# Kernel optimization log

Hardware: AMD Instinct MI355X
Metric: run time of the kernel (lower is better)

The kernel has to match this reference:

```python
import jax, jax.numpy as jnp
import numpy as np

B, G, S, NNZ = 64, 20000, 200000, 2000000

def setup_inputs() -> dict:
    key = jax.random.key(0)
    k1, k2, k3, k4, k5 = jax.random.split(key, 5)
    x = jax.random.normal(k1, (B, G), dtype=jnp.float32)
    # COO connectivity: row = SNP index (output), col = gene index (input)
    row = jax.random.randint(k2, (NNZ,), 0, S, dtype=jnp.int64)
    col = jax.random.randint(k3, (NNZ,), 0, G, dtype=jnp.int64)
    index = jnp.stack([row, col])  # [2, NNZ]
    W_sparse = jax.random.normal(k4, (NNZ,), dtype=jnp.float32) * 0.02
    b = jax.random.normal(k5, (S, 1), dtype=jnp.float32) * 0.02
    return {"x": x, "W_sparse": W_sparse, "b": b, "index": index, "n_SNPs": S}

def reference(x, W_sparse, b, index, n_SNPs):
    # spmm: sparse [n_SNPs, n_genes] @ x.T [n_genes, B] -> [n_SNPs, B]
    row, col = index[0], index[1]
    gathered = x.T[col] * W_sparse[:, None]            # [NNZ, B] edge contributions
    dot_prod = jax.ops.segment_sum(gathered, row, num_segments=n_SNPs)  # [S, B]
    output = dot_prod + b                              # bias broadcast over batch
    return output.T                                    # [B, n_SNPs]
```

## Files before the change

kernel.cpp:

```cpp
#include <hip/hip_runtime.h>


#define WAVE 64
#define CHUNK 8192
#define RBITS 6
#define BINROWS 64
#define SCAN_PAD 3584
#define CAP_BIN 896

#define RL(v, i)  __builtin_amdgcn_readlane((int)(v), (i))
#define RLF(v, i) __int_as_float(__builtin_amdgcn_readlane(__float_as_int(v), (i)))

__device__ __forceinline__ int swz(int r, int b) {
    return (r << 6) + (b ^ (r & 63));
}

__device__ __forceinline__ unsigned short f2bf(float f) {
    unsigned u = __float_as_uint(f);
    unsigned r = (u + 0x7fffu + ((u >> 16) & 1u)) >> 16;
    return (unsigned short)r;
}

__global__ void transpose64_kernel(const float* __restrict__ x,
                                   unsigned short* __restrict__ xTh, int G) {
    __shared__ float tile[64][65];
    const int t  = threadIdx.x;
    const int g0 = blockIdx.x * 64;
    {
        const int j  = t & 63;
        const int b0 = t >> 6;
        if (g0 + j < G) {
            #pragma unroll
            for (int it = 0; it < 16; ++it) {
                const int b = b0 + it * 4;
                tile[j][b] = x[(size_t)b * G + g0 + j];
            }
        }
    }
    __syncthreads();
    {
        const int b  = t & 63;
        const int j0 = t >> 6;
        #pragma unroll
        for (int it = 0; it < 16; ++it) {
            const int j = j0 + it * 4;
            if (g0 + j < G) xTh[(size_t)(g0 + j) * WAVE + b] = f2bf(tile[j][b]);
        }
    }
}

__global__ __launch_bounds__(512) void pass1_kernel(
        const int* __restrict__ row, const int* __restrict__ col,
        const float* __restrict__ w, uint2* __restrict__ sedge1,
        unsigned* __restrict__ segtab, int nnz, int nbin) {
    __shared__ __align__(16) uint2 stage[CHUNK];
    __shared__ int hist[SCAN_PAD];
    __shared__ int wpart[8];
    const int t    = threadIdx.x;
    const int lane = t & 63;
    const int wv   = t >> 6;
    const int e0   = blockIdx.x * CHUNK;
    const bool full = (e0 + CHUNK <= nnz);
    const int M    = full ? CHUNK : (nnz - e0);

    for (int j = t; j < SCAN_PAD; j += 512) hist[j] = 0;
    __syncthreads();

    if (full) {
        const int4* rv = (const int4*)(row + e0);
        #pragma unroll
        for (int k = 0; k < CHUNK / 2048; ++k) {
            const int4 r4 = rv[k * 512 + t];
            atomicAdd(&hist[r4.x >> RBITS], 1);
            atomicAdd(&hist[r4.y >> RBITS], 1);
            atomicAdd(&hist[r4.z >> RBITS], 1);
            atomicAdd(&hist[r4.w >> RBITS], 1);
        }
    } else {
        for (int k = 0; k < CHUNK / 512; ++k) {
            const int i = k * 512 + t;
            if (i < M) atomicAdd(&hist[row[e0 + i] >> RBITS], 1);
        }
    }
    __syncthreads();

    int c[7];
    int p = 0;
    #pragma unroll
    for (int j = 0; j < 7; ++j) { c[j] = hist[t * 7 + j]; p += c[j]; }
    int incl = p;
    #pragma unroll
    for (int d = 1; d < 64; d <<= 1) {
        const int u = __shfl_up(incl, d);
        if (lane >= d) incl += u;
    }
    if (lane == 63) wpart[wv] = incl;
    __syncthreads();
    int base = incl - p;
    #pragma unroll
    for (int ww = 0; ww < 8; ++ww)
        if (ww < wv) base += wpart[ww];
    unsigned* st = segtab + (size_t)blockIdx.x * (size_t)(nbin + 1);
    int run = base;
    #pragma unroll
    for (int j = 0; j < 7; ++j) {
        const int bj = t * 7 + j;
        hist[bj] = run;
        if (bj <= nbin) st[bj] = (unsigned)(e0 + run);
        run += c[j];
    }
    __syncthreads();

    if (full) {
        const int4*   rv = (const int4*)(row + e0);
        const int4*   cv = (const int4*)(col + e0);
        const float4* wf = (const float4*)(w + e0);
        #pragma unroll
        for (int k = 0; k < CHUNK / 2048; ++k) {
            const int4   r4 = rv[k * 512 + t];
            const int4   c4 = cv[k * 512 + t];
            const float4 w4 = wf[k * 512 + t];
            {
                const int pos = atomicAdd(&hist[r4.x >> RBITS], 1);
                stage[pos] = make_uint2(((unsigned)(r4.x & 63) << 15) |
                                        (unsigned)c4.x, __float_as_uint(w4.x));
            }
            {
                const int pos = atomicAdd(&hist[r4.y >> RBITS], 1);
                stage[pos] = make_uint2(((unsigned)(r4.y & 63) << 15) |
                                        (unsigned)c4.y, __float_as_uint(w4.y));
            }
            {
                const int pos = atomicAdd(&hist[r4.z >> RBITS], 1);
                stage[pos] = make_uint2(((unsigned)(r4.z & 63) << 15) |
                                        (unsigned)c4.z, __float_as_uint(w4.z));
            }
            {
                const int pos = atomicAdd(&hist[r4.w >> RBITS], 1);
                stage[pos] = make_uint2(((unsigned)(r4.w & 63) << 15) |
                                        (unsigned)c4.w, __float_as_uint(w4.w));
            }
        }
    } else {
        for (int k = 0; k < CHUNK / 512; ++k) {
            const int i = k * 512 + t;
            if (i < M) {
                const int r = row[e0 + i];
                const int pos = atomicAdd(&hist[r >> RBITS], 1);
                stage[pos] = make_uint2(((unsigned)(r & 63) << 15) |
                                        (unsigned)col[e0 + i],
                                        __float_as_uint(w[e0 + i]));
            }
        }
    }
    __syncthreads();

    {
        const uint4* sg4 = (const uint4*)stage;
        uint4* o4 = (uint4*)(sedge1 + e0);
        for (int j = t; j < (M >> 1); j += 512) o4[j] = sg4[j];
        if ((M & 1) && t == 0) sedge1[e0 + M - 1] = stage[M - 1];
    }
}

#define PROC(Er, ar, ii)                                                      \
    {                                                                         \
        const int   k_ = RL((Er).x, (ii));                                    \
        const float w_ = __int_as_float(RL((Er).y, (ii)));                    \
        const float v_ = __uint_as_float(                                     \
            (unsigned)*(const unsigned short*)(xb + k_ + lane2) << 16);       \
        (ar) += v_ * w_;                                                      \
    }

__global__ __launch_bounds__(256) void compute_kernel(
        const unsigned short* __restrict__ xTh,
        const uint2* __restrict__ sedge1,
        const unsigned* __restrict__ segtab,
        const float* __restrict__ bias,
        float* __restrict__ out, int S, int nchunk, int nbin) {
    __shared__ float tile[64 * 64];
    __shared__ uint2 eds2[CAP_BIN];
    __shared__ int   rcnt[4][BINROWS];
    __shared__ int   cur[4][BINROWS];
    __shared__ int   rstart[BINROWS], rend[BINROWS];
    __shared__ int   spart[4];
    uint2* eds1 = (uint2*)tile;

    const int t    = threadIdx.x;
    const int lane = t & 63;
    const int wv   = t >> 6;

    const int nwg = nbin;
    const int q8 = nwg >> 3, r8 = nwg & 7;
    const int xcd = (int)blockIdx.x & 7, off = (int)blockIdx.x >> 3;
    const int b = (xcd < r8 ? xcd * (q8 + 1) : r8 * (q8 + 1) + (xcd - r8) * q8)
                  + off;
    const int r0 = b << RBITS;

    if (t < BINROWS) {
        rcnt[0][t] = 0; rcnt[1][t] = 0; rcnt[2][t] = 0; rcnt[3][t] = 0;
    }

    int myst0 = 0, myn0 = 0, myst1 = 0, myn1 = 0;
    {
        const size_t stride = (size_t)(nbin + 1);
        if (t < nchunk) {
            const unsigned s = segtab[(size_t)t * stride + b];
            myn0  = (int)(segtab[(size_t)t * stride + b + 1] - s);
            myst0 = (int)s;
        }
        const int c2 = t + 256;
        if (c2 < nchunk) {
            const unsigned s = segtab[(size_t)c2 * stride + b];
            myn1  = (int)(segtab[(size_t)c2 * stride + b + 1] - s);
            myst1 = (int)s;
        }
    }
    const int nt = myn0 + myn1;
    int incl = nt;
    #pragma unroll
    for (int d = 1; d < 64; d <<= 1) {
        const int u = __shfl_up(incl, d);
        if (lane >= d) incl += u;
    }
    if (lane == 63) spart[wv] = incl;
    __syncthreads();
    int base = incl - nt;
    #pragma unroll
    for (int ww = 0; ww < 4; ++ww)
        if (ww < wv) base += spart[ww];
    int M = spart[0] + spart[1] + spart[2] + spart[3];
    if (M > CAP_BIN) M = CAP_BIN;

    for (int k = 0; k < myn0; ++k) {
        const int p = base + k;
        if (p < CAP_BIN) eds1[p] = sedge1[myst0 + k];
    }
    for (int k = 0; k < myn1; ++k) {
        const int p = base + myn0 + k;
        if (p < CAP_BIN) eds1[p] = sedge1[myst1 + k];
    }
    __syncthreads();

    for (int i = t; i < M; i += 256)
        atomicAdd(&rcnt[wv][eds1[i].x >> 15], 1);
    __syncthreads();

    if (t < BINROWS) {
        const int c0 = rcnt[0][t], c1 = rcnt[1][t];
        const int c2 = rcnt[2][t], c3 = rcnt[3][t];
        const int tot = c0 + c1 + c2 + c3;
        int inc2 = tot;
        #pragma unroll
        for (int d = 1; d < 64; d <<= 1) {
            const int u = __shfl_up(inc2, d);
            if (lane >= d) inc2 += u;
        }
        const int stt = inc2 - tot;
        rstart[t] = stt;
        rend[t]   = stt + tot;
        cur[0][t] = stt;
        cur[1][t] = stt + c0;
        cur[2][t] = stt + c0 + c1;
        cur[3][t] = stt + c0 + c1 + c2;
    }
    __syncthreads();

    for (int i = t; i < M; i += 256) {
        const uint2 e = eds1[i];
        const int r = (int)(e.x >> 15);
        const int pos = atomicAdd(&cur[wv][r], 1);
        eds2[pos] = make_uint2((e.x & 0x7fffu) << 7, e.y);
    }
    __syncthreads();

    const char* xb = (const char*)xTh;
    const int lane2 = lane * 2;
    const int rw = r0 + wv * 16;
    float bv = 0.f;
    if (lane < 16 && rw + lane < S) bv = bias[rw + lane];

    #pragma unroll
    for (int qd = 0; qd < 4; ++qd) {
        const int rl = wv * 16 + qd * 4;
        int s0 = rstart[rl + 0], e0g = rend[rl + 0];
        int s1 = rstart[rl + 1], e1g = rend[rl + 1];
        int s2 = rstart[rl + 2], e2g = rend[rl + 2];
        int s3 = rstart[rl + 3], e3g = rend[rl + 3];
        float a0 = 0.f, a1 = 0.f, a2 = 0.f, a3 = 0.f;
        while ((s0 < e0g) || (s1 < e1g) || (s2 < e2g) || (s3 < e3g)) {
            const int m0 = min(WAVE, e0g - s0);
            const int m1 = min(WAVE, e1g - s1);
            const int m2 = min(WAVE, e2g - s2);
            const int m3 = min(WAVE, e3g - s3);
            uint2 E0 = make_uint2(0u, 0u), E1 = make_uint2(0u, 0u);
            uint2 E2 = make_uint2(0u, 0u), E3 = make_uint2(0u, 0u);
            if (lane < m0) E0 = eds2[s0 + lane];
            if (lane < m1) E1 = eds2[s1 + lane];
            if (lane < m2) E2 = eds2[s2 + lane];
            if (lane < m3) E3 = eds2[s3 + lane];
            const int mm = max(max(m0, m1), max(m2, m3));
            int i = 0;
            for (; i + 2 <= mm; i += 2) {
                PROC(E0, a0, i) PROC(E1, a1, i) PROC(E2, a2, i) PROC(E3, a3, i)
                PROC(E0, a0, i + 1) PROC(E1, a1, i + 1)
                PROC(E2, a2, i + 1) PROC(E3, a3, i + 1)
            }
            if (i < mm) {
                PROC(E0, a0, i) PROC(E1, a1, i) PROC(E2, a2, i) PROC(E3, a3, i)
            }
            s0 += max(m0, 0); s1 += max(m1, 0);
            s2 += max(m2, 0); s3 += max(m3, 0);
        }
        tile[swz(rl + 0, lane)] = a0 + RLF(bv, qd * 4 + 0);
        tile[swz(rl + 1, lane)] = a1 + RLF(bv, qd * 4 + 1);
        tile[swz(rl + 2, lane)] = a2 + RLF(bv, qd * 4 + 2);
        tile[swz(rl + 3, lane)] = a3 + RLF(bv, qd * 4 + 3);
    }
    __syncthreads();

    const int srow = r0 + lane;
    #pragma unroll
    for (int k = 0; k < 16; ++k) {
        const int bb = wv * 16 + k;
        if (srow < S) out[(size_t)bb * S + srow] = tile[swz(lane, bb)];
    }
}

extern "C" void kernel_launch(void* const* d_in, const int* in_sizes, int n_in,
                              void* d_out, int out_size, void* d_ws, size_t ws_size,
                              hipStream_t stream) {
    const float* x    = (const float*)d_in[0];
    const float* W    = (const float*)d_in[1];
    const float* bias = (const float*)d_in[2];
    const int*   idx  = (const int*)d_in[3];

    const int NNZ = in_sizes[1];
    const int S   = in_sizes[2];
    const int B   = out_size / S;
    const int G   = in_sizes[0] / B;
    const int* rowi = idx;
    const int* coli = idx + NNZ;
    float* out = (float*)d_out;

    const int nbin   = (S + BINROWS - 1) >> RBITS;
    const int nchunk = (NNZ + CHUNK - 1) / CHUNK;

    char* ws = (char*)d_ws;
    size_t o = 0;
    auto alloc = [&](size_t bytes) {
        void* p = ws + o;
        o = (o + bytes + 255) & ~(size_t)255;
        return p;
    };
    unsigned short* xTh = (unsigned short*)alloc((size_t)G * B * sizeof(unsigned short));
    uint2*    sedge1 = (uint2*)   alloc((size_t)NNZ * sizeof(uint2));
    unsigned* segtab = (unsigned*)alloc((size_t)nchunk * (size_t)(nbin + 1) *
                                        sizeof(unsigned));
    (void)ws_size; (void)n_in;

    const int tgrid = (G + 63) / 64;
    transpose64_kernel<<<tgrid, 256, 0, stream>>>(x, xTh, G);

    pass1_kernel<<<nchunk, 512, 0, stream>>>(rowi, coli, W, sedge1, segtab,
                                             NNZ, nbin);
    compute_kernel<<<nbin, 256, 0, stream>>>(xTh, sedge1, segtab, bias,
                                             out, S, nchunk, nbin);
}
```

Measured before the change: 165.1 us.

## Fuse transpose and binning passes into one launch with smaller chunks

Merges the x transpose/bf16 conversion kernel and the edge-binning pass into a single prep kernel: the first blocks transpose and the rest bin edges, which removes one launch and lets the two run concurrently. Chunk size drops from 8192 to 2048 edges, with 256 threads per block and each thread keeping its row/col/weight loads in registers between the histogram and scatter phases. The result is four times as many chunks, so the compute kernel now reads up to four segment-table entries per thread and gathers from more, smaller segments. That adds scattered segtab reads and shorter copy loops in the compute stage.

```diff
diff --git a/kernel.cpp b/kernel.cpp
--- a/kernel.cpp
+++ b/kernel.cpp
@@ -2,11 +2,12 @@
 
 
 #define WAVE 64
-#define CHUNK 8192
+#define CHUNK 2048
 #define RBITS 6
 #define BINROWS 64
-#define SCAN_PAD 3584
+#define NBIN_PAD 3584
 #define CAP_BIN 896
+#define PREP_SMEM (CHUNK * 8 + NBIN_PAD * 4 + 16)
 
 #define RL(v, i)  __builtin_amdgcn_readlane((int)(v), (i))
 #define RLF(v, i) __int_as_float(__builtin_amdgcn_readlane(__float_as_int(v), (i)))
@@ -21,145 +22,138 @@
     return (unsigned short)r;
 }
 
-__global__ void transpose64_kernel(const float* __restrict__ x,
-                                   unsigned short* __restrict__ xTh, int G) {
-    __shared__ float tile[64][65];
-    const int t  = threadIdx.x;
-    const int g0 = blockIdx.x * 64;
-    {
-        const int j  = t & 63;
-        const int b0 = t >> 6;
-        if (g0 + j < G) {
-            #pragma unroll
-            for (int it = 0; it < 16; ++it) {
-                const int b = b0 + it * 4;
-                tile[j][b] = x[(size_t)b * G + g0 + j];
-            }
-        }
-    }
-    __syncthreads();
-    {
-        const int b  = t & 63;
-        const int j0 = t >> 6;
-        #pragma unroll
-        for (int it = 0; it < 16; ++it) {
-            const int j = j0 + it * 4;
-            if (g0 + j < G) xTh[(size_t)(g0 + j) * WAVE + b] = f2bf(tile[j][b]);
-        }
-    }
-}
-
-__global__ __launch_bounds__(512) void pass1_kernel(
+__global__ __launch_bounds__(256) void prep_kernel(
+        const float* __restrict__ x, unsigned short* __restrict__ xTh,
+        int G, int tgrid,
         const int* __restrict__ row, const int* __restrict__ col,
         const float* __restrict__ w, uint2* __restrict__ sedge1,
         unsigned* __restrict__ segtab, int nnz, int nbin) {
-    __shared__ __align__(16) uint2 stage[CHUNK];
-    __shared__ int hist[SCAN_PAD];
-    __shared__ int wpart[8];
-    const int t    = threadIdx.x;
+    __shared__ __align__(16) char smem[PREP_SMEM];
+    const int t = threadIdx.x;
+
+    if ((int)blockIdx.x < tgrid) {
+        float (*tile)[65] = (float (*)[65])smem;
+        const int g0 = blockIdx.x * 64;
+        {
+            const int j  = t & 63;
+            const int b0 = t >> 6;
+            if (g0 + j < G) {
+                #pragma unroll
+                for (int it = 0; it < 16; ++it) {
+                    const int b = b0 + it * 4;
+                    tile[j][b] = x[(size_t)b * G + g0 + j];
+                }
+            }
+        }
+        __syncthreads();
+        {
+            const int b  = t & 63;
+            const int j0 = t >> 6;
+            #pragma unroll
+            for (int it = 0; it < 16; ++it) {
+                const int j = j0 + it * 4;
+                if (g0 + j < G) xTh[(size_t)(g0 + j) * WAVE + b] = f2bf(tile[j][b]);
+            }
+        }
+        return;
+    }
+
+    uint2* stage = (uint2*)smem;
+    int*   hist  = (int*)(smem + CHUNK * 8);
+    int*   wpart = (int*)(smem + CHUNK * 8 + NBIN_PAD * 4);
     const int lane = t & 63;
     const int wv   = t >> 6;
-    const int e0   = blockIdx.x * CHUNK;
+    const int blk  = (int)blockIdx.x - tgrid;
+    const int e0   = blk * CHUNK;
     const bool full = (e0 + CHUNK <= nnz);
     const int M    = full ? CHUNK : (nnz - e0);
 
-    for (int j = t; j < SCAN_PAD; j += 512) hist[j] = 0;
-    __syncthreads();
-
-    if (full) {
-        const int4* rv = (const int4*)(row + e0);
-        #pragma unroll
-        for (int k = 0; k < CHUNK / 2048; ++k) {
-            const int4 r4 = rv[k * 512 + t];
-            atomicAdd(&hist[r4.x >> RBITS], 1);
-            atomicAdd(&hist[r4.y >> RBITS], 1);
-            atomicAdd(&hist[r4.z >> RBITS], 1);
-            atomicAdd(&hist[r4.w >> RBITS], 1);
-        }
-    } else {
-        for (int k = 0; k < CHUNK / 512; ++k) {
-            const int i = k * 512 + t;
-            if (i < M) atomicAdd(&hist[row[e0 + i] >> RBITS], 1);
-        }
-    }
-    __syncthreads();
-
-    int c[7];
-    int p = 0;
-    #pragma unroll
-    for (int j = 0; j < 7; ++j) { c[j] = hist[t * 7 + j]; p += c[j]; }
-    int incl = p;
-    #pragma unroll
-    for (int d = 1; d < 64; d <<= 1) {
-        const int u = __shfl_up(incl, d);
-        if (lane >= d) incl += u;
-    }
-    if (lane == 63) wpart[wv] = incl;
-    __syncthreads();
-    int base = incl - p;
-    #pragma unroll
-    for (int ww = 0; ww < 8; ++ww)
-        if (ww < wv) base += wpart[ww];
-    unsigned* st = segtab + (size_t)blockIdx.x * (size_t)(nbin + 1);
-    int run = base;
-    #pragma unroll
-    for (int j = 0; j < 7; ++j) {
-        const int bj = t * 7 + j;
-        hist[bj] = run;
-        if (bj <= nbin) st[bj] = (unsigned)(e0 + run);
-        run += c[j];
-    }
-    __syncthreads();
-
+    for (int j = t; j < NBIN_PAD; j += 256) hist[j] = 0;
+    __syncthreads();
+
+    int4 ra, rb, ca, cb; float4 wa, wb;
     if (full) {
         const int4*   rv = (const int4*)(row + e0);
         const int4*   cv = (const int4*)(col + e0);
         const float4* wf = (const float4*)(w + e0);
-        #pragma unroll
-        for (int k = 0; k < CHUNK / 2048; ++k) {
-            const int4   r4 = rv[k * 512 + t];
-            const int4   c4 = cv[k * 512 + t];
-            const float4 w4 = wf[k * 512 + t];
-            {
-                const int pos = atomicAdd(&hist[r4.x >> RBITS], 1);
-                stage[pos] = make_uint2(((unsigned)(r4.x & 63) << 15) |
-                                        (unsigned)c4.x, __float_as_uint(w4.x));
-            }
-            {
-                const int pos = atomicAdd(&hist[r4.y >> RBITS], 1);
-                stage[pos] = make_uint2(((unsigned)(r4.y & 63) << 15) |
-                                        (unsigned)c4.y, __float_as_uint(w4.y));
-            }
-            {
-                const int pos = atomicAdd(&hist[r4.z >> RBITS], 1);
-                stage[pos] = make_uint2(((unsigned)(r4.z & 63) << 15) |
-                                        (unsigned)c4.z, __float_as_uint(w4.z));
-            }
-            {
-                const int pos = atomicAdd(&hist[r4.w >> RBITS], 1);
-                stage[pos] = make_uint2(((unsigned)(r4.w & 63) << 15) |
-                                        (unsigned)c4.w, __float_as_uint(w4.w));
-            }
-        }
+        ra = rv[t]; rb = rv[t + 256];
+        ca = cv[t]; cb = cv[t + 256];
+        wa = wf[t]; wb = wf[t + 256];
+        atomicAdd(&hist[ra.x >> RBITS], 1);
+        atomicAdd(&hist[ra.y >> RBITS], 1);
+        atomicAdd(&hist[ra.z >> RBITS], 1);
+        atomicAdd(&hist[ra.w >> RBITS], 1);
+        atomicAdd(&hist[rb.x >> RBITS], 1);
+        atomicAdd(&hist[rb.y >> RBITS], 1);
+        atomicAdd(&hist[rb.z >> RBITS], 1);
+        atomicAdd(&hist[rb.w >> RBITS], 1);
     } else {
-        for (int k = 0; k < CHUNK / 512; ++k) {
-            const int i = k * 512 + t;
+        for (int k = 0; k < CHUNK / 256; ++k) {
+            const int i = k * 256 + t;
+            if (i < M) atomicAdd(&hist[row[e0 + i] >> RBITS], 1);
+        }
+    }
+    __syncthreads();
+
+    {
+        int c[14];
+        int p = 0;
+        #pragma unroll
+        for (int j = 0; j < 14; ++j) { c[j] = hist[t * 14 + j]; p += c[j]; }
+        int incl = p;
+        #pragma unroll
+        for (int d = 1; d < 64; d <<= 1) {
+            const int u = __shfl_up(incl, d);
+            if (lane >= d) incl += u;
+        }
+        if (lane == 63) wpart[wv] = incl;
+        __syncthreads();
+        int base = incl - p;
+        #pragma unroll
+        for (int ww = 0; ww < 4; ++ww)
+            if (ww < wv) base += wpart[ww];
+        unsigned* st = segtab + (size_t)blk * (size_t)(nbin + 1);
+        int run = base;
+        #pragma unroll
+        for (int j = 0; j < 14; ++j) {
+            const int bj = t * 14 + j;
+            hist[bj] = run;
+            if (bj <= nbin) st[bj] = (unsigned)(e0 + run);
+            run += c[j];
+        }
+    }
+    __syncthreads();
+
+#define PUT(r_, c_, w_)                                                       \
+    {                                                                         \
+        const int pos = atomicAdd(&hist[(r_) >> RBITS], 1);                   \
+        stage[pos] = make_uint2(((unsigned)((r_) & 63) << 15) |               \
+                                (unsigned)(c_), __float_as_uint(w_));         \
+    }
+    if (full) {
+        PUT(ra.x, ca.x, wa.x) PUT(ra.y, ca.y, wa.y)
+        PUT(ra.z, ca.z, wa.z) PUT(ra.w, ca.w, wa.w)
+        PUT(rb.x, cb.x, wb.x) PUT(rb.y, cb.y, wb.y)
+        PUT(rb.z, cb.z, wb.z) PUT(rb.w, cb.w, wb.w)
+    } else {
+        for (int k = 0; k < CHUNK / 256; ++k) {
+            const int i = k * 256 + t;
             if (i < M) {
                 const int r = row[e0 + i];
-                const int pos = atomicAdd(&hist[r >> RBITS], 1);
-                stage[pos] = make_uint2(((unsigned)(r & 63) << 15) |
-                                        (unsigned)col[e0 + i],
-                                        __float_as_uint(w[e0 + i]));
-            }
-        }
-    }
-    __syncthreads();
-
-    {
+                PUT(r, col[e0 + i], w[e0 + i])
+            }
+        }
+    }
+#undef PUT
+    __syncthreads();
+
+    if (full) {
         const uint4* sg4 = (const uint4*)stage;
         uint4* o4 = (uint4*)(sedge1 + e0);
-        for (int j = t; j < (M >> 1); j += 512) o4[j] = sg4[j];
-        if ((M & 1) && t == 0) sedge1[e0 + M - 1] = stage[M - 1];
+        #pragma unroll
+        for (int k = 0; k < CHUNK / 512; ++k) o4[k * 256 + t] = sg4[k * 256 + t];
+    } else {
+        for (int j = t; j < M; j += 256) sedge1[e0 + j] = stage[j];
     }
 }
 
@@ -201,22 +195,27 @@
         rcnt[0][t] = 0; rcnt[1][t] = 0; rcnt[2][t] = 0; rcnt[3][t] = 0;
     }
 
-    int myst0 = 0, myn0 = 0, myst1 = 0, myn1 = 0;
+    int st0 = 0, n0_ = 0, st1 = 0, n1_ = 0, st2 = 0, n2_ = 0, st3 = 0, n3_ = 0;
     {
         const size_t stride = (size_t)(nbin + 1);
         if (t < nchunk) {
-            const unsigned s = segtab[(size_t)t * stride + b];
-            myn0  = (int)(segtab[(size_t)t * stride + b + 1] - s);
-            myst0 = (int)s;
-        }
-        const int c2 = t + 256;
-        if (c2 < nchunk) {
-            const unsigned s = segtab[(size_t)c2 * stride + b];
-            myn1  = (int)(segtab[(size_t)c2 * stride + b + 1] - s);
-            myst1 = (int)s;
-        }
-    }
-    const int nt = myn0 + myn1;
+            const unsigned* p = segtab + (size_t)t * stride + b;
+            st0 = (int)p[0]; n0_ = (int)(p[1] - p[0]);
+        }
+        if (t + 256 < nchunk) {
+            const unsigned* p = segtab + (size_t)(t + 256) * stride + b;
+            st1 = (int)p[0]; n1_ = (int)(p[1] - p[0]);
+        }
+        if (t + 512 < nchunk) {
+            const unsigned* p = segtab + (size_t)(t + 512) * stride + b;
+            st2 = (int)p[0]; n2_ = (int)(p[1] - p[0]);
+        }
+        if (t + 768 < nchunk) {
+            const unsigned* p = segtab + (size_t)(t + 768) * stride + b;
+            st3 = (int)p[0]; n3_ = (int)(p[1] - p[0]);
+        }
+    }
+    const int nt = n0_ + n1_ + n2_ + n3_;
     int incl = nt;
     #pragma unroll
     for (int d = 1; d < 64; d <<= 1) {
@@ -232,13 +231,16 @@
     int M = spart[0] + spart[1] + spart[2] + spart[3];
     if (M > CAP_BIN) M = CAP_BIN;
 
-    for (int k = 0; k < myn0; ++k) {
-        const int p = base + k;
-        if (p < CAP_BIN) eds1[p] = sedge1[myst0 + k];
-    }
-    for (int k = 0; k < myn1; ++k) {
-        const int p = base + myn0 + k;
-        if (p < CAP_BIN) eds1[p] = sedge1[myst1 + k];
+    {
+        int p = base;
+        for (int k = 0; k < n0_; ++k, ++p)
+            if (p < CAP_BIN) eds1[p] = sedge1[st0 + k];
+        for (int k = 0; k < n1_; ++k, ++p)
+            if (p < CAP_BIN) eds1[p] = sedge1[st1 + k];
+        for (int k = 0; k < n2_; ++k, ++p)
+            if (p < CAP_BIN) eds1[p] = sedge1[st2 + k];
+        for (int k = 0; k < n3_; ++k, ++p)
+            if (p < CAP_BIN) eds1[p] = sedge1[st3 + k];
     }
     __syncthreads();
 
@@ -345,6 +347,7 @@
 
     const int nbin   = (S + BINROWS - 1) >> RBITS;
     const int nchunk = (NNZ + CHUNK - 1) / CHUNK;
+    const int tgrid  = (G + 63) / 64;
 
     char* ws = (char*)d_ws;
     size_t o = 0;
@@ -359,11 +362,9 @@
                                         sizeof(unsigned));
     (void)ws_size; (void)n_in;
 
-    const int tgrid = (G + 63) / 64;
-    transpose64_kernel<<<tgrid, 256, 0, stream>>>(x, xTh, G);
-
-    pass1_kernel<<<nchunk, 512, 0, stream>>>(rowi, coli, W, sedge1, segtab,
-                                             NNZ, nbin);
+    prep_kernel<<<tgrid + nchunk, 256, 0, stream>>>(
+        x, xTh, G, tgrid, rowi, coli, W, sedge1, segtab, NNZ, nbin);
+
     compute_kernel<<<nbin, 256, 0, stream>>>(xTh, sedge1, segtab, bias,
                                              out, S, nchunk, nbin);
 }
```

Measured after the change: 179.3 us. +8.6%, slower.

## Shrink row bins to 32 and accumulate per-wave LDS tiles without row sorting

Applied to the files above, without the earlier changes.

Row bins shrink from 64 to 32 rows, so pass1 now builds a larger histogram of 13 bins per thread. The compute kernel drops the in-block counting sort by row. Each wave now takes 64-edge batches, with each half-wave handling one edge at a time, and gathers two bf16 batch values per lane. It accumulates into a private per-wave 32x64 LDS tile and sums the four tiles plus bias at output time. This removes the sort phase and the per-row load imbalance, at the cost of LDS read-modify-write per edge, more bins and blocks, and a larger pass1 scan.

```diff
diff --git a/kernel.cpp b/kernel.cpp
--- a/kernel.cpp
+++ b/kernel.cpp
@@ -3,17 +3,12 @@
 
 #define WAVE 64
 #define CHUNK 8192
-#define RBITS 6
-#define BINROWS 64
-#define SCAN_PAD 3584
-#define CAP_BIN 896
+#define RBITS 5
+#define BINROWS 32
+#define NBIN_PAD 6656
+#define CAP_BIN 576
 
 #define RL(v, i)  __builtin_amdgcn_readlane((int)(v), (i))
-#define RLF(v, i) __int_as_float(__builtin_amdgcn_readlane(__float_as_int(v), (i)))
-
-__device__ __forceinline__ int swz(int r, int b) {
-    return (r << 6) + (b ^ (r & 63));
-}
 
 __device__ __forceinline__ unsigned short f2bf(float f) {
     unsigned u = __float_as_uint(f);
@@ -54,7 +49,7 @@
         const float* __restrict__ w, uint2* __restrict__ sedge1,
         unsigned* __restrict__ segtab, int nnz, int nbin) {
     __shared__ __align__(16) uint2 stage[CHUNK];
-    __shared__ int hist[SCAN_PAD];
+    __shared__ int hist[NBIN_PAD];
     __shared__ int wpart[8];
     const int t    = threadIdx.x;
     const int lane = t & 63;
@@ -63,7 +58,7 @@
     const bool full = (e0 + CHUNK <= nnz);
     const int M    = full ? CHUNK : (nnz - e0);
 
-    for (int j = t; j < SCAN_PAD; j += 512) hist[j] = 0;
+    for (int j = t; j < NBIN_PAD; j += 512) hist[j] = 0;
     __syncthreads();
 
     if (full) {
@@ -84,30 +79,32 @@
     }
     __syncthreads();
 
-    int c[7];
-    int p = 0;
-    #pragma unroll
-    for (int j = 0; j < 7; ++j) { c[j] = hist[t * 7 + j]; p += c[j]; }
-    int incl = p;
-    #pragma unroll
-    for (int d = 1; d < 64; d <<= 1) {
-        const int u = __shfl_up(incl, d);
-        if (lane >= d) incl += u;
-    }
-    if (lane == 63) wpart[wv] = incl;
-    __syncthreads();
-    int base = incl - p;
-    #pragma unroll
-    for (int ww = 0; ww < 8; ++ww)
-        if (ww < wv) base += wpart[ww];
-    unsigned* st = segtab + (size_t)blockIdx.x * (size_t)(nbin + 1);
-    int run = base;
-    #pragma unroll
-    for (int j = 0; j < 7; ++j) {
-        const int bj = t * 7 + j;
-        hist[bj] = run;
-        if (bj <= nbin) st[bj] = (unsigned)(e0 + run);
-        run += c[j];
+    {
+        int c[13];
+        int p = 0;
+        #pragma unroll
+        for (int j = 0; j < 13; ++j) { c[j] = hist[t * 13 + j]; p += c[j]; }
+        int incl = p;
+        #pragma unroll
+        for (int d = 1; d < 64; d <<= 1) {
+            const int u = __shfl_up(incl, d);
+            if (lane >= d) incl += u;
+        }
+        if (lane == 63) wpart[wv] = incl;
+        __syncthreads();
+        int base = incl - p;
+        #pragma unroll
+        for (int ww = 0; ww < 8; ++ww)
+            if (ww < wv) base += wpart[ww];
+        unsigned* st = segtab + (size_t)blockIdx.x * (size_t)(nbin + 1);
+        int run = base;
+        #pragma unroll
+        for (int j = 0; j < 13; ++j) {
+            const int bj = t * 13 + j;
+            hist[bj] = run;
+            if (bj <= nbin) st[bj] = (unsigned)(e0 + run);
+            run += c[j];
+        }
     }
     __syncthreads();
 
@@ -122,22 +119,22 @@
             const float4 w4 = wf[k * 512 + t];
             {
                 const int pos = atomicAdd(&hist[r4.x >> RBITS], 1);
-                stage[pos] = make_uint2(((unsigned)(r4.x & 63) << 15) |
+                stage[pos] = make_uint2(((unsigned)(r4.x & (BINROWS - 1)) << 15) |
                                         (unsigned)c4.x, __float_as_uint(w4.x));
             }
             {
                 const int pos = atomicAdd(&hist[r4.y >> RBITS], 1);
-                stage[pos] = make_uint2(((unsigned)(r4.y & 63) << 15) |
+                stage[pos] = make_uint2(((unsigned)(r4.y & (BINROWS - 1)) << 15) |
                                         (unsigned)c4.y, __float_as_uint(w4.y));
             }
             {
                 const int pos = atomicAdd(&hist[r4.z >> RBITS], 1);
-                stage[pos] = make_uint2(((unsigned)(r4.z & 63) << 15) |
+                stage[pos] = make_uint2(((unsigned)(r4.z & (BINROWS - 1)) << 15) |
                                         (unsigned)c4.z, __float_as_uint(w4.z));
             }
             {
                 const int pos = atomicAdd(&hist[r4.w >> RBITS], 1);
-                stage[pos] = make_uint2(((unsigned)(r4.w & 63) << 15) |
+                stage[pos] = make_uint2(((unsigned)(r4.w & (BINROWS - 1)) << 15) |
                                         (unsigned)c4.w, __float_as_uint(w4.w));
             }
         }
@@ -147,7 +144,7 @@
             if (i < M) {
                 const int r = row[e0 + i];
                 const int pos = atomicAdd(&hist[r >> RBITS], 1);
-                stage[pos] = make_uint2(((unsigned)(r & 63) << 15) |
+                stage[pos] = make_uint2(((unsigned)(r & (BINROWS - 1)) << 15) |
                                         (unsigned)col[e0 + i],
                                         __float_as_uint(w[e0 + i]));
             }
@@ -162,15 +159,6 @@
         if ((M & 1) && t == 0) sedge1[e0 + M - 1] = stage[M - 1];
     }
 }
-
-#define PROC(Er, ar, ii)                                                      \
-    {                                                                         \
-        const int   k_ = RL((Er).x, (ii));                                    \
-        const float w_ = __int_as_float(RL((Er).y, (ii)));                    \
-        const float v_ = __uint_as_float(                                     \
-            (unsigned)*(const unsigned short*)(xb + k_ + lane2) << 16);       \
-        (ar) += v_ * w_;                                                      \
-    }
 
 __global__ __launch_bounds__(256) void compute_kernel(
         const unsigned short* __restrict__ xTh,
@@ -178,46 +166,35 @@
         const unsigned* __restrict__ segtab,
         const float* __restrict__ bias,
         float* __restrict__ out, int S, int nchunk, int nbin) {
-    __shared__ float tile[64 * 64];
-    __shared__ uint2 eds2[CAP_BIN];
-    __shared__ int   rcnt[4][BINROWS];
-    __shared__ int   cur[4][BINROWS];
-    __shared__ int   rstart[BINROWS], rend[BINROWS];
+    __shared__ float tiles[4 * 2048];
+    __shared__ uint2 eds[CAP_BIN];
     __shared__ int   spart[4];
-    uint2* eds1 = (uint2*)tile;
 
     const int t    = threadIdx.x;
     const int lane = t & 63;
     const int wv   = t >> 6;
-
-    const int nwg = nbin;
-    const int q8 = nwg >> 3, r8 = nwg & 7;
+    const int l31  = lane & 31;
+    const int half = lane >> 5;
+
+    const int q8 = nbin >> 3, r8 = nbin & 7;
     const int xcd = (int)blockIdx.x & 7, off = (int)blockIdx.x >> 3;
     const int b = (xcd < r8 ? xcd * (q8 + 1) : r8 * (q8 + 1) + (xcd - r8) * q8)
                   + off;
     const int r0 = b << RBITS;
 
-    if (t < BINROWS) {
-        rcnt[0][t] = 0; rcnt[1][t] = 0; rcnt[2][t] = 0; rcnt[3][t] = 0;
-    }
-
-    int myst0 = 0, myn0 = 0, myst1 = 0, myn1 = 0;
-    {
-        const size_t stride = (size_t)(nbin + 1);
-        if (t < nchunk) {
-            const unsigned s = segtab[(size_t)t * stride + b];
-            myn0  = (int)(segtab[(size_t)t * stride + b + 1] - s);
-            myst0 = (int)s;
-        }
-        const int c2 = t + 256;
-        if (c2 < nchunk) {
-            const unsigned s = segtab[(size_t)c2 * stride + b];
-            myn1  = (int)(segtab[(size_t)c2 * stride + b + 1] - s);
-            myst1 = (int)s;
-        }
-    }
-    const int nt = myn0 + myn1;
-    int incl = nt;
+    {
+        float4* tz = (float4*)(tiles + wv * 2048);
+        #pragma unroll
+        for (int k = 0; k < 8; ++k) tz[k * 64 + lane] = make_float4(0, 0, 0, 0);
+    }
+
+    int st = 0, cnt = 0;
+    if (t < nchunk) {
+        const unsigned* p = segtab + (size_t)t * (size_t)(nbin + 1) + b;
+        const unsigned s0 = p[0];
+        st = (int)s0; cnt = (int)(p[1] - s0);
+    }
+    int incl = cnt;
     #pragma unroll
     for (int d = 1; d < 64; d <<= 1) {
         const int u = __shfl_up(incl, d);
@@ -225,105 +202,70 @@
     }
     if (lane == 63) spart[wv] = incl;
     __syncthreads();
-    int base = incl - nt;
+    int base = incl - cnt;
     #pragma unroll
     for (int ww = 0; ww < 4; ++ww)
         if (ww < wv) base += spart[ww];
     int M = spart[0] + spart[1] + spart[2] + spart[3];
     if (M > CAP_BIN) M = CAP_BIN;
 
-    for (int k = 0; k < myn0; ++k) {
-        const int p = base + k;
-        if (p < CAP_BIN) eds1[p] = sedge1[myst0 + k];
-    }
-    for (int k = 0; k < myn1; ++k) {
-        const int p = base + myn0 + k;
-        if (p < CAP_BIN) eds1[p] = sedge1[myst1 + k];
-    }
-    __syncthreads();
-
-    for (int i = t; i < M; i += 256)
-        atomicAdd(&rcnt[wv][eds1[i].x >> 15], 1);
-    __syncthreads();
-
-    if (t < BINROWS) {
-        const int c0 = rcnt[0][t], c1 = rcnt[1][t];
-        const int c2 = rcnt[2][t], c3 = rcnt[3][t];
-        const int tot = c0 + c1 + c2 + c3;
-        int inc2 = tot;
-        #pragma unroll
-        for (int d = 1; d < 64; d <<= 1) {
-            const int u = __shfl_up(inc2, d);
-            if (lane >= d) inc2 += u;
-        }
-        const int stt = inc2 - tot;
-        rstart[t] = stt;
-        rend[t]   = stt + tot;
-        cur[0][t] = stt;
-        cur[1][t] = stt + c0;
-        cur[2][t] = stt + c0 + c1;
-        cur[3][t] = stt + c0 + c1 + c2;
-    }
-    __syncthreads();
-
-    for (int i = t; i < M; i += 256) {
-        const uint2 e = eds1[i];
-        const int r = (int)(e.x >> 15);
-        const int pos = atomicAdd(&cur[wv][r], 1);
-        eds2[pos] = make_uint2((e.x & 0x7fffu) << 7, e.y);
-    }
-    __syncthreads();
-
-    const char* xb = (const char*)xTh;
-    const int lane2 = lane * 2;
-    const int rw = r0 + wv * 16;
-    float bv = 0.f;
-    if (lane < 16 && rw + lane < S) bv = bias[rw + lane];
-
+    for (int k = 0; k < cnt; ++k) {
+        const int pp = base + k;
+        if (pp < CAP_BIN) eds[pp] = sedge1[st + k];
+    }
+    const int Mp = (M + 63) & ~63;
+    if (t < Mp - M) eds[M + t] = make_uint2(0u, 0u);
+    __syncthreads();
+
+    const char* xbl = (const char*)xTh + l31 * 4;
+    float* T = tiles + wv * 2048;
+    const int nb64 = Mp >> 6;
+    for (int bt = wv; bt < nb64; bt += 4) {
+        const uint2 E = eds[bt * 64 + lane];
+        #pragma unroll
+        for (int j = 0; j < 32; ++j) {
+            const int kA = RL(E.x, 2 * j),  kB = RL(E.x, 2 * j + 1);
+            const int wA = RL(E.y, 2 * j),  wB = RL(E.y, 2 * j + 1);
+            const int key   = half ? kB : kA;
+            const float w   = __int_as_float(half ? wB : wA);
+            const int rA = kA >> 15, rB = kB >> 15;
+            const int r  = half ? rB : rA;
+            const unsigned cb = ((unsigned)key & 0x7fffu) << 7;
+            const unsigned d  = *(const unsigned*)(xbl + cb);
+            const float vlo = __uint_as_float(d << 16);
+            const float vhi = __uint_as_float(d & 0xffff0000u);
+            const float clo = vlo * w, chi = vhi * w;
+            float* tp = T + (r << 6) + ((l31 ^ r) << 1);
+            if (rA != rB) {
+                float2 acc = *(float2*)tp;
+                acc.x += clo; acc.y += chi;
+                *(float2*)tp = acc;
+            } else {
+                const float plo = __shfl_xor(clo, 32);
+                const float phi = __shfl_xor(chi, 32);
+                if (half == 0) {
+                    float2 acc = *(float2*)tp;
+                    acc.x += clo + plo; acc.y += chi + phi;
+                    *(float2*)tp = acc;
+                }
+            }
+        }
+    }
+    __syncthreads();
+
+    const int rr = l31;
+    float bvr = 0.f;
+    const bool rok = (r0 + rr < S);
+    if (rok) bvr = bias[r0 + rr];
     #pragma unroll
-    for (int qd = 0; qd < 4; ++qd) {
-        const int rl = wv * 16 + qd * 4;
-        int s0 = rstart[rl + 0], e0g = rend[rl + 0];
-        int s1 = rstart[rl + 1], e1g = rend[rl + 1];
-        int s2 = rstart[rl + 2], e2g = rend[rl + 2];
-        int s3 = rstart[rl + 3], e3g = rend[rl + 3];
-        float a0 = 0.f, a1 = 0.f, a2 = 0.f, a3 = 0.f;
-        while ((s0 < e0g) || (s1 < e1g) || (s2 < e2g) || (s3 < e3g)) {
-            const int m0 = min(WAVE, e0g - s0);
-            const int m1 = min(WAVE, e1g - s1);
-            const int m2 = min(WAVE, e2g - s2);
-            const int m3 = min(WAVE, e3g - s3);
-            uint2 E0 = make_uint2(0u, 0u), E1 = make_uint2(0u, 0u);
-            uint2 E2 = make_uint2(0u, 0u), E3 = make_uint2(0u, 0u);
-            if (lane < m0) E0 = eds2[s0 + lane];
-            if (lane < m1) E1 = eds2[s1 + lane];
-            if (lane < m2) E2 = eds2[s2 + lane];
-            if (lane < m3) E3 = eds2[s3 + lane];
-            const int mm = max(max(m0, m1), max(m2, m3));
-            int i = 0;
-            for (; i + 2 <= mm; i += 2) {
-                PROC(E0, a0, i) PROC(E1, a1, i) PROC(E2, a2, i) PROC(E3, a3, i)
-                PROC(E0, a0, i + 1) PROC(E1, a1, i + 1)
-                PROC(E2, a2, i + 1) PROC(E3, a3, i + 1)
-            }
-            if (i < mm) {
-                PROC(E0, a0, i) PROC(E1, a1, i) PROC(E2, a2, i) PROC(E3, a3, i)
-            }
-            s0 += max(m0, 0); s1 += max(m1, 0);
-            s2 += max(m2, 0); s3 += max(m3, 0);
-        }
-        tile[swz(rl + 0, lane)] = a0 + RLF(bv, qd * 4 + 0);
-        tile[swz(rl + 1, lane)] = a1 + RLF(bv, qd * 4 + 1);
-        tile[swz(rl + 2, lane)] = a2 + RLF(bv, qd * 4 + 2);
-        tile[swz(rl + 3, lane)] = a3 + RLF(bv, qd * 4 + 3);
-    }
-    __syncthreads();
-
-    const int srow = r0 + lane;
-    #pragma unroll
-    for (int k = 0; k < 16; ++k) {
-        const int bb = wv * 16 + k;
-        if (srow < S) out[(size_t)bb * S + srow] = tile[swz(lane, bb)];
+    for (int k = 0; k < 8; ++k) {
+        const int bb  = wv * 16 + k * 2 + half;
+        const int p   = bb >> 1;
+        const int sub = bb & 1;
+        const int o   = (rr << 6) + ((p ^ rr) << 1) + sub;
+        float v = tiles[o] + tiles[2048 + o] + tiles[4096 + o] + tiles[6144 + o]
+                + bvr;
+        if (rok) out[(size_t)bb * S + r0 + rr] = v;
     }
 }
 
```

After: 245.0 us. 48.5% more time.
